# Performance work log

Hardware: AMD Instinct MI355X
Metric: run time of the kernel (lower is better)

The kernel has to match this reference:

```python
import jax, jax.numpy as jnp
import numpy as np

NUM_HEADS = 16
HEAD_DIM = 128
ROPE_BASE = 10000.0


def _rotate_half(x):
    x1, x2 = jnp.split(x, 2, axis=-1)
    return jnp.concatenate([-x2, x1], axis=-1)


def setup_inputs() -> dict:
    key = jax.random.key(0)
    ks = jax.random.split(key, 6)
    B, S, H = 2, 2048, 2048
    hidden_states = jax.random.normal(ks[0], (B, S, H), dtype=jnp.float32)
    # causal additive mask: 0 on/below diagonal, large negative above
    causal = jnp.tril(jnp.ones((S, S), dtype=bool))
    attention_mask = jnp.where(causal, 0.0, -1e9).astype(jnp.float32)[None, None]
    position_ids = jnp.broadcast_to(jnp.arange(S, dtype=jnp.int64), (B, S))
    sc = 1.0 / np.sqrt(H)
    Wq = jax.random.normal(ks[1], (H, H), dtype=jnp.float32) * sc
    Wk = jax.random.normal(ks[2], (H, H), dtype=jnp.float32) * sc
    Wv = jax.random.normal(ks[3], (H, H), dtype=jnp.float32) * sc
    Wo = jax.random.normal(ks[4], (H, H), dtype=jnp.float32) * sc
    return {"hidden_states": hidden_states, "attention_mask": attention_mask,
            "position_ids": position_ids, "Wq": Wq, "Wk": Wk, "Wv": Wv, "Wo": Wo}


def reference(hidden_states, attention_mask, position_ids, Wq, Wk, Wv, Wo):
    B, S, H = hidden_states.shape
    nH, hd = NUM_HEADS, HEAD_DIM
    # projections (torch Linear: x @ W.T)
    q = (hidden_states @ Wq.T).reshape(B, S, nH, hd).transpose(0, 2, 1, 3)  # [B,nH,S,hd]
    k = (hidden_states @ Wk.T).reshape(B, S, nH, hd).transpose(0, 2, 1, 3)
    v = (hidden_states @ Wv.T).reshape(B, S, nH, hd).transpose(0, 2, 1, 3)
    # rotary embeddings: cos/sin cache over positions, duplicated to full head_dim
    inv_freq = 1.0 / (ROPE_BASE ** (jnp.arange(0, hd, 2, dtype=jnp.float32) / hd))  # [hd/2]
    t = jnp.arange(S, dtype=jnp.float32)
    freqs = jnp.outer(t, inv_freq)                       # [S, hd/2]
    emb = jnp.concatenate([freqs, freqs], axis=-1)       # [S, hd]
    cos = jnp.cos(emb)[position_ids][:, None]            # [B,1,S,hd]
    sin = jnp.sin(emb)[position_ids][:, None]
    q = q * cos + _rotate_half(q) * sin
    k = k * cos + _rotate_half(k) * sin
    # eager attention
    scores = jnp.einsum('bhqd,bhkd->bhqk', q, k) / np.sqrt(hd).astype(np.float32)
    scores = scores + attention_mask
    attn = jax.nn.softmax(scores, axis=-1)
    out = jnp.einsum('bhqk,bhkd->bhqd', attn, v)         # [B,nH,S,hd]
    out = out.transpose(0, 2, 1, 3).reshape(B, S, H)
    return out @ Wo.T
```

## Files before the change

### kernel.cpp

```cpp
#include <hip/hip_runtime.h>
#include <cstdint>
#include <cstddef>

#define NH    16
#define HD    128
#define SEQ   2048
#define HID   2048
#define BATCH 2
#define MTOT  (BATCH*SEQ)

#define SCALE 0.08838834764831845f
#define L2E   1.4426950408889634f
#define KSCL  (0.08838834764831845f * 1.4426950408889634f)
#define L2_10K_D64 0.20762050593046458f

typedef __bf16 bf16x8 __attribute__((ext_vector_type(8)));
typedef float  floatx4 __attribute__((ext_vector_type(4)));

__device__ __forceinline__ unsigned short f2bf(float f) {
  union { float f; unsigned u; } v; v.f = f;
  unsigned u = v.u;
  return (unsigned short)((u + 0x7FFFu + ((u >> 16) & 1u)) >> 16);
}
__device__ __forceinline__ float bf2f(unsigned short h) {
  union { unsigned u; float f; } v; v.u = ((unsigned)h) << 16; return v.f;
}

__device__ __forceinline__ void gld16(const unsigned short* g, unsigned short* l) {
  auto gp = reinterpret_cast<const __attribute__((address_space(1))) void*>(
      reinterpret_cast<uintptr_t>(g));
  auto lp = reinterpret_cast<__attribute__((address_space(3))) void*>(
      reinterpret_cast<uintptr_t>(l));
  __builtin_amdgcn_global_load_lds(gp, lp, 16, 0, 0);
}

__global__ void rope_tab(float2* __restrict__ T) {
  int idx = blockIdx.x * blockDim.x + threadIdx.x;
  int s = idx >> 6, i = idx & 63;
  float freq = exp2f(-(float)i * L2_10K_D64);
  float th = (float)s * freq;
  T[idx] = make_float2(cosf(th), sinf(th));
}

__global__ void cvt_all(const float* __restrict__ X,
                        const float* __restrict__ Wq, const float* __restrict__ Wk,
                        const float* __restrict__ Wv, const float* __restrict__ Wo,
                        unsigned short* __restrict__ Xb,
                        unsigned short* __restrict__ Wqb, unsigned short* __restrict__ Wkb,
                        unsigned short* __restrict__ Wvb, unsigned short* __restrict__ Wob) {
  int i = blockIdx.x * blockDim.x + threadIdx.x;
  const float* src; unsigned short* dst; int k;
  if (i < (1 << 21)) { src = X; dst = Xb; k = i; }
  else {
    int j = i - (1 << 21);
    int seg = j >> 20; k = j & ((1 << 20) - 1);
    src = (seg == 0) ? Wq : (seg == 1) ? Wk : (seg == 2) ? Wv : Wo;
    dst = (seg == 0) ? Wqb : (seg == 1) ? Wkb : (seg == 2) ? Wvb : Wob;
  }
  float4 v = reinterpret_cast<const float4*>(src)[k];
  ushort4 o;
  o.x = f2bf(v.x); o.y = f2bf(v.y); o.z = f2bf(v.z); o.w = f2bf(v.w);
  reinterpret_cast<ushort4*>(dst)[k] = o;
}


#define SBAR      asm volatile("s_barrier" ::: "memory")
#define WAITLGKM  asm volatile("s_waitcnt lgkmcnt(0)" ::: "memory")
#define WAITVM(n) asm volatile("s_waitcnt vmcnt(" #n ")" ::: "memory")
#define PRIO1     __builtin_amdgcn_s_setprio(1)
#define PRIO0     __builtin_amdgcn_s_setprio(0)
#define SCHED0    __builtin_amdgcn_sched_barrier(0)

#define STAGE_A(p, t8)                                                          \
  {                                                                             \
    int row_ = tid >> 2, g_ = tid & 3;                                          \
    gld16(Ag + (size_t)row_ * HID + (t8) * 32 + ((g_ ^ (row_ & 3)) * 8),        \
          As + (p) * 4096 + tid * 8);                                           \
  }

#define STAGE_B(p, t8)                                                          \
  {                                                                             \
    _Pragma("unroll")                                                           \
    for (int j_ = 0; j_ < 2; ++j_) {                                            \
      int G_ = j_ * 512 + tid;                                                  \
      int row_ = G_ >> 2, g_ = G_ & 3;                                          \
      gld16(Bg + (size_t)row_ * HID + (t8) * 32 + ((g_ ^ (row_ & 3)) * 8),      \
            Bs + (p) * 8192 + G_ * 8);                                          \
    }                                                                           \
  }

#define READS(p)                                                                \
  _Pragma("unroll")                                                             \
  for (int mr_ = 0; mr_ < 4; ++mr_)                                             \
    af[mr_] = *reinterpret_cast<const bf16x8*>(                                 \
        &As[(p) * 4096 + (wm * 64 + mr_ * 16 + l16) * 32 + cg]);                \
  _Pragma("unroll")                                                             \
  for (int nr_ = 0; nr_ < 4; ++nr_)                                             \
    bfr[nr_] = *reinterpret_cast<const bf16x8*>(                                \
        &Bs[(p) * 8192 + (nr_ * 64 + wn * 16 + l16) * 32 + cg]);

#define MMH(h)                                                                  \
  _Pragma("unroll")                                                             \
  for (int mr_ = 0; mr_ < 4; ++mr_)                                             \
    _Pragma("unroll")                                                           \
    for (int nr_ = 0; nr_ < 2; ++nr_)                                           \
      acc[mr_][(h) * 2 + nr_] = __builtin_amdgcn_mfma_f32_16x16x32_bf16(        \
          af[mr_], bfr[(h) * 2 + nr_], acc[mr_][(h) * 2 + nr_], 0, 0, 0);

__global__ __launch_bounds__(512, 4)
void gemm_qkv32(const unsigned short* __restrict__ Xb,
                const unsigned short* __restrict__ Wq,
                const unsigned short* __restrict__ Wk,
                const unsigned short* __restrict__ Wv,
                const float2* __restrict__ ropeT,
                unsigned short* __restrict__ Qo,
                unsigned short* __restrict__ Ko,
                unsigned short* __restrict__ Vto) {
  __shared__ unsigned short As[2 * 4096];
  __shared__ unsigned short Bs[2 * 8192];

  const int bid = blockIdx.x;
  const int xcd = bid & 7;
  const int j   = bid >> 3;
  const int zn  = xcd * 3 + (j >> 5);
  const int by  = j & 31;
  const int z   = zn >> 3;
  const int bx  = zn & 7;

  const unsigned short* W = (z == 0) ? Wq : (z == 1) ? Wk : Wv;
  const int mBase = by * 128, nBase = bx * 256;
  const unsigned short* Ag = Xb + (size_t)mBase * HID;
  const unsigned short* Bg = W  + (size_t)nBase * HID;

  const int tid  = threadIdx.x;
  const int wave = tid >> 6, lane = tid & 63;
  const int l16  = lane & 15, quad = lane >> 4;
  const int wm   = wave >> 2, wn = wave & 3;
  const int cg   = (quad ^ (l16 & 3)) * 8;

  floatx4 acc[4][4];
#pragma unroll
  for (int i = 0; i < 4; ++i)
#pragma unroll
    for (int jj = 0; jj < 4; ++jj) acc[i][jj] = {0.f, 0.f, 0.f, 0.f};

  bf16x8 af[4], bfr[4];

  STAGE_A(0, 0); STAGE_B(0, 0);
  STAGE_A(1, 1); STAGE_B(1, 1);
  WAITVM(3);
  SBAR;

#pragma unroll 1
  for (int i = 0; i < 31; ++i) {
    const int t = 2 * i;
    READS(0);
    WAITLGKM; SCHED0; PRIO1; MMH(0); PRIO0; SBAR;
    STAGE_A(0, t + 2); STAGE_B(0, t + 2);
    SCHED0; PRIO1; MMH(1); PRIO0; WAITVM(3); SBAR;
    READS(1);
    WAITLGKM; SCHED0; PRIO1; MMH(0); PRIO0; SBAR;
    STAGE_A(1, t + 3); STAGE_B(1, t + 3);
    SCHED0; PRIO1; MMH(1); PRIO0; WAITVM(3); SBAR;
  }
  READS(0);
  WAITLGKM; SCHED0; PRIO1; MMH(0); PRIO0; SBAR;
  SCHED0; PRIO1; MMH(1); PRIO0; WAITVM(0); SBAR;
  READS(1);
  WAITLGKM; SCHED0; PRIO1; MMH(0); MMH(1); PRIO0;

  if (z < 2) {
    unsigned short* dst = (z == 0) ? Qo : Ko;
    const int hh0 = nBase >> 7;
    const int d1  = wn * 16 + l16;
#pragma unroll
    for (int mr = 0; mr < 4; ++mr) {
      int srow = mBase + wm * 64 + mr * 16 + quad * 4;
      int bb = srow >> 11, s = srow & (SEQ - 1);
#pragma unroll
      for (int r = 0; r < 4; ++r) {
        float2 cs = ropeT[(size_t)(s + r) * 64 + d1];
#pragma unroll
        for (int p = 0; p < 2; ++p) {
          float x1 = acc[mr][2 * p][r], x2 = acc[mr][2 * p + 1][r];
          size_t base = (((size_t)bb * NH + hh0 + p) * SEQ + (s + r)) * HD;
          dst[base + d1]      = f2bf(x1 * cs.x - x2 * cs.y);
          dst[base + d1 + 64] = f2bf(x2 * cs.x + x1 * cs.y);
        }
      }
    }
  } else {
#pragma unroll
    for (int mr = 0; mr < 4; ++mr) {
      int mrow = mBase + wm * 64 + mr * 16 + quad * 4;
      int bb = mrow >> 11, s = mrow & (SEQ - 1);
#pragma unroll
      for (int nr = 0; nr < 4; ++nr) {
        int n = nBase + nr * 64 + wn * 16 + l16;
        int hh = n >> 7, d = n & 127;
        ushort4 pk;
        pk.x = f2bf(acc[mr][nr][0]); pk.y = f2bf(acc[mr][nr][1]);
        pk.z = f2bf(acc[mr][nr][2]); pk.w = f2bf(acc[mr][nr][3]);
        *reinterpret_cast<ushort4*>(&Vto[(((size_t)bb * NH + hh) * HD + d) * SEQ + s]) = pk;
      }
    }
  }
}

__device__ __forceinline__ void gemm_core(const unsigned short* __restrict__ A,
                                          const unsigned short* __restrict__ B,
                                          int K, int mBase, int nBase,
                                          unsigned short* As, unsigned short* Bs,
                                          floatx4 acc[4][4]) {
  int tid  = threadIdx.x;
  int wave = tid >> 6, lane = tid & 63;
  int l16  = lane & 15, quad = lane >> 4;
  int wm   = wave >> 1, wn = wave & 1;

  const unsigned short* Ag = A + (size_t)mBase * K;
  const unsigned short* Bg = B + (size_t)nBase * K;

  for (int k0 = 0; k0 < K; k0 += 32) {
    __syncthreads();
#pragma unroll
    for (int r = 0; r < 2; ++r) {
      int row0 = wave * 32 + r * 16;
      int grow = row0 + (lane >> 2);
      int gcol = k0 + (lane & 3) * 8;
      gld16(Ag + (size_t)grow * K + gcol, As + row0 * 32 + lane * 8);
      gld16(Bg + (size_t)grow * K + gcol, Bs + row0 * 32 + lane * 8);
    }
    __syncthreads();

    bf16x8 af[4], bfr[4];
#pragma unroll
    for (int t = 0; t < 4; ++t) {
      af[t]  = *reinterpret_cast<const bf16x8*>(&As[(wm * 64 + t * 16 + l16) * 32 + quad * 8]);
      bfr[t] = *reinterpret_cast<const bf16x8*>(&Bs[(wn * 64 + t * 16 + l16) * 32 + quad * 8]);
    }
#pragma unroll
    for (int tm = 0; tm < 4; ++tm)
#pragma unroll
      for (int tn = 0; tn < 4; ++tn)
        acc[tm][tn] = __builtin_amdgcn_mfma_f32_16x16x32_bf16(af[tm], bfr[tn], acc[tm][tn], 0, 0, 0);
  }
}

__global__ __launch_bounds__(256)
void gemm_out(const unsigned short* __restrict__ Ob,
              const unsigned short* __restrict__ Wo,
              float* __restrict__ out) {
  __shared__ unsigned short As[128 * 32];
  __shared__ unsigned short Bs[128 * 32];
  int mBase = blockIdx.y * 128, nBase = blockIdx.x * 128;

  floatx4 acc[4][4];
#pragma unroll
  for (int i = 0; i < 4; ++i)
#pragma unroll
    for (int j = 0; j < 4; ++j) acc[i][j] = {0.f, 0.f, 0.f, 0.f};

  gemm_core(Ob, Wo, HID, mBase, nBase, As, Bs, acc);

  int tid = threadIdx.x;
  int wave = tid >> 6, lane = tid & 63;
  int l16 = lane & 15, quad = lane >> 4;
  int wm = wave >> 1, wn = wave & 1;

#pragma unroll
  for (int tm = 0; tm < 4; ++tm) {
    int mrow = mBase + wm * 64 + tm * 16 + quad * 4;
#pragma unroll
    for (int tn = 0; tn < 4; ++tn) {
      int n = nBase + wn * 64 + tn * 16 + l16;
#pragma unroll
      for (int r = 0; r < 4; ++r)
        out[(size_t)(mrow + r) * HID + n] = acc[tm][tn][r];
    }
  }
}

__global__ __launch_bounds__(512)
void attn_kernel(const unsigned short* __restrict__ Q,
                 const unsigned short* __restrict__ K,
                 const unsigned short* __restrict__ Vt,
                 unsigned short* __restrict__ Ob) {
  __shared__ unsigned short Ks[32 * 136];
  __shared__ unsigned short Vs[128 * 40];
  __shared__ unsigned short Ps[8][16 * 40];

  int qt = 15 - blockIdx.y;
  int bh = blockIdx.x;
  int b = bh >> 4, h = bh & 15;
  int q0 = qt * 128;
  int tid = threadIdx.x;
  int wave = tid >> 6, lane = tid & 63;
  int l16 = lane & 15, quad = lane >> 4;

  const size_t headQ = (size_t)bh * SEQ * HD;
  const size_t headV = (size_t)bh * HD * SEQ;

  bf16x8 qf[4];
  {
    int qrow = q0 + wave * 16 + l16;
    const unsigned short* qp = Q + headQ + (size_t)qrow * HD + quad * 8;
#pragma unroll
    for (int c = 0; c < 4; ++c)
      qf[c] = *reinterpret_cast<const bf16x8*>(qp + c * 32);
  }

  floatx4 oacc[8];
#pragma unroll
  for (int i = 0; i < 8; ++i) oacc[i] = {0.f, 0.f, 0.f, 0.f};
  float rs[4];
#pragma unroll
  for (int r = 0; r < 4; ++r) rs[r] = 0.f;

  int qq = q0 + wave * 16 + quad * 4;
  int qmax = q0 + wave * 16 + 15;
  unsigned short* pw = Ps[wave];

  const int krow = tid >> 4, kdc = (tid & 15) * 8;
  const int vrow = tid >> 2, vkc = (tid & 3) * 8;

  int nkt = q0 / 32 + 4;

  uint4 kreg = *reinterpret_cast<const uint4*>(&K[headQ + (size_t)krow * HD + kdc]);
  uint4 vreg = *reinterpret_cast<const uint4*>(&Vt[headV + (size_t)vrow * SEQ + vkc]);

  for (int kt = 0; kt < nkt; ++kt) {
    int k0 = kt * 32;
    __syncthreads();
    *reinterpret_cast<uint4*>(&Ks[krow * 136 + kdc]) = kreg;
    *reinterpret_cast<uint4*>(&Vs[vrow * 40 + vkc]) = vreg;
    int k0n = (kt + 1 < nkt) ? (k0 + 32) : k0;
    kreg = *reinterpret_cast<const uint4*>(&K[headQ + (size_t)(k0n + krow) * HD + kdc]);
    vreg = *reinterpret_cast<const uint4*>(&Vt[headV + (size_t)vrow * SEQ + k0n + vkc]);
    __syncthreads();

    if (k0 <= qmax) {
      floatx4 sc[2];
#pragma unroll
      for (int nt = 0; nt < 2; ++nt) {
        floatx4 s4 = {0.f, 0.f, 0.f, 0.f};
#pragma unroll
        for (int c = 0; c < 4; ++c) {
          bf16x8 kf = *reinterpret_cast<const bf16x8*>(&Ks[(nt * 16 + l16) * 136 + c * 32 + quad * 8]);
          s4 = __builtin_amdgcn_mfma_f32_16x16x32_bf16(qf[c], kf, s4, 0, 0, 0);
        }
        sc[nt] = s4;
      }

#pragma unroll
      for (int nt = 0; nt < 2; ++nt) {
        int kk = k0 + nt * 16 + l16;
#pragma unroll
        for (int r = 0; r < 4; ++r) {
          float arg = (kk <= qq + r) ? fmaf(sc[nt][r], KSCL, -32.0f) : -1e9f;
          float p = exp2f(arg);
          rs[r] += p;
          pw[(quad * 4 + r) * 40 + nt * 16 + l16] = f2bf(p);
        }
      }
      __asm__ __volatile__("s_waitcnt lgkmcnt(0)" ::: "memory");
      bf16x8 pf = *reinterpret_cast<const bf16x8*>(&pw[l16 * 40 + quad * 8]);

#pragma unroll
      for (int dt = 0; dt < 8; ++dt) {
        bf16x8 vf = *reinterpret_cast<const bf16x8*>(&Vs[(dt * 16 + l16) * 40 + quad * 8]);
        oacc[dt] = __builtin_amdgcn_mfma_f32_16x16x32_bf16(pf, vf, oacc[dt], 0, 0, 0);
      }
    }
  }

#pragma unroll
  for (int off = 1; off < 16; off <<= 1)
#pragma unroll
    for (int r = 0; r < 4; ++r) rs[r] += __shfl_xor(rs[r], off, 16);

  float inv[4];
#pragma unroll
  for (int r = 0; r < 4; ++r) inv[r] = 1.0f / rs[r];
#pragma unroll
  for (int dt = 0; dt < 8; ++dt)
#pragma unroll
    for (int r = 0; r < 4; ++r) {
      int s = q0 + wave * 16 + quad * 4 + r;
      Ob[(((size_t)b * SEQ + s) * NH + h) * HD + dt * 16 + l16] = f2bf(oacc[dt][r] * inv[r]);
    }
}

extern "C" void kernel_launch(void* const* d_in, const int* in_sizes, int n_in,
                              void* d_out, int out_size, void* d_ws, size_t ws_size,
                              hipStream_t stream) {
  const float* X  = (const float*)d_in[0];
  const float* Wq = (const float*)d_in[3];
  const float* Wk = (const float*)d_in[4];
  const float* Wv = (const float*)d_in[5];
  const float* Wo = (const float*)d_in[6];

  char* w = (char*)d_ws;
  size_t off = 0;
  auto alloc = [&](size_t bytes) { char* p = w + off; off += (bytes + 255) & ~(size_t)255; return p; };

  unsigned short* Xb  = (unsigned short*)alloc((size_t)MTOT * HID * 2);
  unsigned short* Wqb = (unsigned short*)alloc((size_t)HID * HID * 2);
  unsigned short* Wkb = (unsigned short*)alloc((size_t)HID * HID * 2);
  unsigned short* Wvb = (unsigned short*)alloc((size_t)HID * HID * 2);
  unsigned short* Wob = (unsigned short*)alloc((size_t)HID * HID * 2);
  unsigned short* Qb  = (unsigned short*)alloc((size_t)BATCH * NH * SEQ * HD * 2);
  unsigned short* Kb  = (unsigned short*)alloc((size_t)BATCH * NH * SEQ * HD * 2);
  unsigned short* Vtb = (unsigned short*)alloc((size_t)BATCH * NH * HD * SEQ * 2);
  unsigned short* Obf = (unsigned short*)alloc((size_t)BATCH * SEQ * NH * HD * 2);
  float2*         ropeT = (float2*)alloc((size_t)SEQ * 64 * sizeof(float2));

  rope_tab<<<(SEQ * 64) / 256, 256, 0, stream>>>(ropeT);

  const int nAll4 = (MTOT * HID + 4 * HID * HID) / 4;
  cvt_all<<<nAll4 / 256, 256, 0, stream>>>(X, Wq, Wk, Wv, Wo, Xb, Wqb, Wkb, Wvb, Wob);

  gemm_qkv32<<<768, 512, 0, stream>>>(Xb, Wqb, Wkb, Wvb, ropeT, Qb, Kb, Vtb);

  attn_kernel<<<dim3(BATCH * NH, SEQ / 128), 512, 0, stream>>>(Qb, Kb, Vtb, Obf);

  gemm_out<<<dim3(HID / 128, MTOT / 128), 256, 0, stream>>>(Obf, Wob, (float*)d_out);
}
```

Measured before the change: 382.8 us.

## Double attention key tile to 64 and reswizzle GEMM LDS layout

The attention kernel now handles 64 keys per iteration instead of 32. That halves the number of loop iterations and __syncthreads pairs, and it doubles the MFMA work done between barriers. Separately, the QKV GEMM's LDS staging layout packs two 32-wide K rows per 64-element line with an 8-way XOR swizzle. This is meant to cut LDS bank conflicts on the fragment reads. The costs are more registers and LDS in attention, and coarser causal masking, which wastes some work on the diagonal tiles.

```diff
diff --git a/kernel.cpp b/kernel.cpp
--- a/kernel.cpp
+++ b/kernel.cpp
@@ -73,8 +73,8 @@
 
 #define STAGE_A(p, t8)                                                          \
   {                                                                             \
-    int row_ = tid >> 2, g_ = tid & 3;                                          \
-    gld16(Ag + (size_t)row_ * HID + (t8) * 32 + ((g_ ^ (row_ & 3)) * 8),        \
+    int r_ = tid >> 3, hx_ = (tid & 7) ^ (r_ & 7);                              \
+    gld16(Ag + (size_t)(2 * r_ + (hx_ >> 2)) * HID + (t8) * 32 + (hx_ & 3) * 8, \
           As + (p) * 4096 + tid * 8);                                           \
   }
 
@@ -83,8 +83,8 @@
     _Pragma("unroll")                                                           \
     for (int j_ = 0; j_ < 2; ++j_) {                                            \
       int G_ = j_ * 512 + tid;                                                  \
-      int row_ = G_ >> 2, g_ = G_ & 3;                                          \
-      gld16(Bg + (size_t)row_ * HID + (t8) * 32 + ((g_ ^ (row_ & 3)) * 8),      \
+      int r_ = G_ >> 3, hx_ = (G_ & 7) ^ (r_ & 7);                              \
+      gld16(Bg + (size_t)(2 * r_ + (hx_ >> 2)) * HID + (t8) * 32 + (hx_ & 3) * 8, \
             Bs + (p) * 8192 + G_ * 8);                                          \
     }                                                                           \
   }
@@ -93,11 +93,11 @@
   _Pragma("unroll")                                                             \
   for (int mr_ = 0; mr_ < 4; ++mr_)                                             \
     af[mr_] = *reinterpret_cast<const bf16x8*>(                                 \
-        &As[(p) * 4096 + (wm * 64 + mr_ * 16 + l16) * 32 + cg]);                \
+        &As[(p) * 4096 + wm * 2048 + mr_ * 512 + lbase]);                       \
   _Pragma("unroll")                                                             \
   for (int nr_ = 0; nr_ < 4; ++nr_)                                             \
     bfr[nr_] = *reinterpret_cast<const bf16x8*>(                                \
-        &Bs[(p) * 8192 + (nr_ * 64 + wn * 16 + l16) * 32 + cg]);
+        &Bs[(p) * 8192 + nr_ * 2048 + wn * 512 + lbase]);
 
 #define MMH(h)                                                                  \
   _Pragma("unroll")                                                             \
@@ -136,7 +136,7 @@
   const int wave = tid >> 6, lane = tid & 63;
   const int l16  = lane & 15, quad = lane >> 4;
   const int wm   = wave >> 2, wn = wave & 3;
-  const int cg   = (quad ^ (l16 & 3)) * 8;
+  const int lbase = (l16 >> 1) * 64 + ((((l16 & 1) << 2) + quad) ^ (l16 >> 1)) * 8;
 
   floatx4 acc[4][4];
 #pragma unroll
@@ -285,9 +285,9 @@
                  const unsigned short* __restrict__ K,
                  const unsigned short* __restrict__ Vt,
                  unsigned short* __restrict__ Ob) {
-  __shared__ unsigned short Ks[32 * 136];
-  __shared__ unsigned short Vs[128 * 40];
-  __shared__ unsigned short Ps[8][16 * 40];
+  __shared__ unsigned short Ks[64 * 136];
+  __shared__ unsigned short Vs[128 * 72];
+  __shared__ unsigned short Ps[8][16 * 72];
 
   int qt = 15 - blockIdx.y;
   int bh = blockIdx.x;
@@ -320,28 +320,35 @@
   int qmax = q0 + wave * 16 + 15;
   unsigned short* pw = Ps[wave];
 
-  const int krow = tid >> 4, kdc = (tid & 15) * 8;
-  const int vrow = tid >> 2, vkc = (tid & 3) * 8;
-
-  int nkt = q0 / 32 + 4;
-
-  uint4 kreg = *reinterpret_cast<const uint4*>(&K[headQ + (size_t)krow * HD + kdc]);
-  uint4 vreg = *reinterpret_cast<const uint4*>(&Vt[headV + (size_t)vrow * SEQ + vkc]);
+  const int kr0 = tid >> 4, kdc = (tid & 15) * 8;
+  const int vr0 = tid >> 3, vkc = (tid & 7) * 8;
+
+  int nkt = q0 / 64 + 2;
+
+  uint4 kreg[2], vreg[2];
+  kreg[0] = *reinterpret_cast<const uint4*>(&K[headQ + (size_t)kr0 * HD + kdc]);
+  kreg[1] = *reinterpret_cast<const uint4*>(&K[headQ + (size_t)(kr0 + 32) * HD + kdc]);
+  vreg[0] = *reinterpret_cast<const uint4*>(&Vt[headV + (size_t)vr0 * SEQ + vkc]);
+  vreg[1] = *reinterpret_cast<const uint4*>(&Vt[headV + (size_t)(vr0 + 64) * SEQ + vkc]);
 
   for (int kt = 0; kt < nkt; ++kt) {
-    int k0 = kt * 32;
+    int k0 = kt * 64;
     __syncthreads();
-    *reinterpret_cast<uint4*>(&Ks[krow * 136 + kdc]) = kreg;
-    *reinterpret_cast<uint4*>(&Vs[vrow * 40 + vkc]) = vreg;
-    int k0n = (kt + 1 < nkt) ? (k0 + 32) : k0;
-    kreg = *reinterpret_cast<const uint4*>(&K[headQ + (size_t)(k0n + krow) * HD + kdc]);
-    vreg = *reinterpret_cast<const uint4*>(&Vt[headV + (size_t)vrow * SEQ + k0n + vkc]);
+    *reinterpret_cast<uint4*>(&Ks[kr0 * 136 + kdc]) = kreg[0];
+    *reinterpret_cast<uint4*>(&Ks[(kr0 + 32) * 136 + kdc]) = kreg[1];
+    *reinterpret_cast<uint4*>(&Vs[vr0 * 72 + vkc]) = vreg[0];
+    *reinterpret_cast<uint4*>(&Vs[(vr0 + 64) * 72 + vkc]) = vreg[1];
+    int k0n = (kt + 1 < nkt) ? (k0 + 64) : k0;
+    kreg[0] = *reinterpret_cast<const uint4*>(&K[headQ + (size_t)(k0n + kr0) * HD + kdc]);
+    kreg[1] = *reinterpret_cast<const uint4*>(&K[headQ + (size_t)(k0n + kr0 + 32) * HD + kdc]);
+    vreg[0] = *reinterpret_cast<const uint4*>(&Vt[headV + (size_t)vr0 * SEQ + k0n + vkc]);
+    vreg[1] = *reinterpret_cast<const uint4*>(&Vt[headV + (size_t)(vr0 + 64) * SEQ + k0n + vkc]);
     __syncthreads();
 
     if (k0 <= qmax) {
-      floatx4 sc[2];
-#pragma unroll
-      for (int nt = 0; nt < 2; ++nt) {
+      floatx4 sc[4];
+#pragma unroll
+      for (int nt = 0; nt < 4; ++nt) {
         floatx4 s4 = {0.f, 0.f, 0.f, 0.f};
 #pragma unroll
         for (int c = 0; c < 4; ++c) {
@@ -352,24 +359,29 @@
       }
 
 #pragma unroll
-      for (int nt = 0; nt < 2; ++nt) {
+      for (int nt = 0; nt < 4; ++nt) {
         int kk = k0 + nt * 16 + l16;
 #pragma unroll
         for (int r = 0; r < 4; ++r) {
           float arg = (kk <= qq + r) ? fmaf(sc[nt][r], KSCL, -32.0f) : -1e9f;
           float p = exp2f(arg);
           rs[r] += p;
-          pw[(quad * 4 + r) * 40 + nt * 16 + l16] = f2bf(p);
+          pw[(quad * 4 + r) * 72 + nt * 16 + l16] = f2bf(p);
         }
       }
       __asm__ __volatile__("s_waitcnt lgkmcnt(0)" ::: "memory");
-      bf16x8 pf = *reinterpret_cast<const bf16x8*>(&pw[l16 * 40 + quad * 8]);
-
-#pragma unroll
-      for (int dt = 0; dt < 8; ++dt) {
-        bf16x8 vf = *reinterpret_cast<const bf16x8*>(&Vs[(dt * 16 + l16) * 40 + quad * 8]);
-        oacc[dt] = __builtin_amdgcn_mfma_f32_16x16x32_bf16(pf, vf, oacc[dt], 0, 0, 0);
-      }
+      bf16x8 pf[2];
+#pragma unroll
+      for (int ks = 0; ks < 2; ++ks)
+        pf[ks] = *reinterpret_cast<const bf16x8*>(&pw[l16 * 72 + ks * 32 + quad * 8]);
+
+#pragma unroll
+      for (int dt = 0; dt < 8; ++dt)
+#pragma unroll
+        for (int ks = 0; ks < 2; ++ks) {
+          bf16x8 vf = *reinterpret_cast<const bf16x8*>(&Vs[(dt * 16 + l16) * 72 + ks * 32 + quad * 8]);
+          oacc[dt] = __builtin_amdgcn_mfma_f32_16x16x32_bf16(pf[ks], vf, oacc[dt], 0, 0, 0);
+        }
     }
   }
 
```

Measured after the change: 463.8 us. 21.2% more time.
